# Performance work log

Hardware: AMD Instinct MI355X
Metric: run time of the kernel (lower is better)

## Reference

```python
import jax, jax.numpy as jnp
import numpy as np

DIM = 2048
STATE = 16
BATCH = 2
SEQ = 2048
LN_EPS = 1e-5


def setup_inputs() -> dict:
    key = jax.random.key(0)
    ks = jax.random.split(key, 12)
    d, n = DIM, STATE
    inp = {
        "x": jax.random.normal(ks[0], (BATCH, SEQ, d), dtype=jnp.float32),
        "ln_gamma": jnp.ones((d,), dtype=jnp.float32),
        "ln_beta": jnp.zeros((d,), dtype=jnp.float32),
        # proj_in: Linear(d, 2d) (spectral-normed; weights treated as effective)
        "W_in": jax.random.normal(ks[1], (2 * d, d), dtype=jnp.float32) / np.sqrt(d),
        "b_in": jnp.zeros((2 * d,), dtype=jnp.float32),
        "state_A": jax.random.normal(ks[2], (n, d), dtype=jnp.float32) * 0.01,
        "W_B": jax.random.normal(ks[3], (n, d), dtype=jnp.float32) / np.sqrt(d),
        "b_B": jnp.zeros((n,), dtype=jnp.float32),
        "W_C": jax.random.normal(ks[4], (n, d), dtype=jnp.float32) / np.sqrt(d),
        "b_C": jnp.zeros((n,), dtype=jnp.float32),
        "W_dt": jax.random.normal(ks[5], (d, d), dtype=jnp.float32) / np.sqrt(d),
        "b_dt": jnp.zeros((d,), dtype=jnp.float32),
        "W_out": jax.random.normal(ks[6], (d, d), dtype=jnp.float32) / np.sqrt(d),
        "b_out": jnp.zeros((d,), dtype=jnp.float32),
    }
    return inp


def reference(x, ln_gamma, ln_beta, W_in, b_in, state_A, W_B, b_B, W_C, b_C,
              W_dt, b_dt, W_out, b_out):
    residual = x
    # LayerNorm over last dim
    mu = jnp.mean(x, axis=-1, keepdims=True)
    var = jnp.mean(jnp.square(x - mu), axis=-1, keepdims=True)
    xn = (x - mu) * jax.lax.rsqrt(var + LN_EPS) * ln_gamma + ln_beta
    # input projection and gate split
    xz = jnp.einsum('bsd,ed->bse', xn, W_in) + b_in          # (B,S,2D)
    x_ssm, z = jnp.split(xz, 2, axis=-1)                      # (B,S,D) each
    # dt = clamp(softplus(proj_dt(x_ssm)), max=1.0)
    dt = jnp.minimum(jax.nn.softplus(jnp.einsum('bsd,ed->bse', x_ssm, W_dt) + b_dt), 1.0)
    Bm = jnp.einsum('bsd,nd->bsn', x_ssm, W_B) + b_B          # (B,S,N)
    Cm = jnp.einsum('bsd,nd->bsn', x_ssm, W_C) + b_C          # (B,S,N)
    # A_bar[b,s,n,d] = exp(state_A[n,d] * dt[b,s,d])
    A_bar = jnp.exp(state_A[None, None, :, :] * dt[:, :, None, :])  # (B,S,N,D)
    # y[b,s,d] = sum_n C[b,s,n]*B[b,s,n]*A_bar[b,s,n,d] * x_ssm[b,s,d]
    y = jnp.einsum('bsn,bsnd->bsd', Cm * Bm, A_bar) * x_ssm
    gated = y * jax.nn.silu(z)
    out = jnp.einsum('bsd,ed->bse', gated, W_out) + b_out
    return out + residual
```

## Files before the change

kernel.cpp:

```cpp
#include <hip/hip_runtime.h>

typedef unsigned short u16;
typedef float f32x4 __attribute__((ext_vector_type(4)));
typedef __bf16 bf16x8 __attribute__((ext_vector_type(8)));

__device__ __forceinline__ u16 f2bf(float f) {
    unsigned u = __float_as_uint(f);
    u += 0x7FFFu + ((u >> 16) & 1u);
    return (u16)(u >> 16);
}
__device__ __forceinline__ float b2f(u16 h) {
    return __uint_as_float(((unsigned)h) << 16);
}

__device__ __forceinline__ void async16(const u16* g, u16* l) {
    __builtin_amdgcn_global_load_lds(
        (__attribute__((address_space(1))) void*)(u16*)g,
        (__attribute__((address_space(3))) void*)l,
        16, 0, 0);
}

#define T_TOK 4096
#define DIM   2048

__global__ __launch_bounds__(256) void castln_kernel(const float* __restrict__ W_in,
                                                     u16* __restrict__ wb_in,
                                                     const float* __restrict__ x,
                                                     const float* __restrict__ g,
                                                     const float* __restrict__ b,
                                                     u16* __restrict__ o) {
    __shared__ float s1[4], s2[4];
    int blk = blockIdx.x, tid = threadIdx.x;
    if (blk < 8192) {
        int i = blk * 256 + tid;
        float4 f = ((const float4*)W_in)[i];
        ushort4 u;
        u.x = f2bf(f.x); u.y = f2bf(f.y); u.z = f2bf(f.z); u.w = f2bf(f.w);
        ((ushort4*)wb_in)[i] = u;
        return;
    }
    int t = blk - 8192;
    int wave = tid >> 6, lane = tid & 63;
    size_t base = (size_t)t * DIM;
    int d0 = tid * 8;
    float4 v0 = *(const float4*)(x + base + d0);
    float4 v1 = *(const float4*)(x + base + d0 + 4);
    float v[8] = {v0.x, v0.y, v0.z, v0.w, v1.x, v1.y, v1.z, v1.w};
    float s = 0.f;
#pragma unroll
    for (int j = 0; j < 8; ++j) s += v[j];
#pragma unroll
    for (int o2 = 32; o2; o2 >>= 1) s += __shfl_xor(s, o2);
    if (lane == 0) s1[wave] = s;
    __syncthreads();
    float mu = (s1[0] + s1[1] + s1[2] + s1[3]) * (1.f / DIM);
    float q = 0.f;
#pragma unroll
    for (int j = 0; j < 8; ++j) { float dd = v[j] - mu; q += dd * dd; }
#pragma unroll
    for (int o2 = 32; o2; o2 >>= 1) q += __shfl_xor(q, o2);
    if (lane == 0) s2[wave] = q;
    __syncthreads();
    float var = (s2[0] + s2[1] + s2[2] + s2[3]) * (1.f / DIM);
    float rs = rsqrtf(var + 1e-5f);
    float4 g0 = *(const float4*)(g + d0), g1 = *(const float4*)(g + d0 + 4);
    float4 b0 = *(const float4*)(b + d0), b1 = *(const float4*)(b + d0 + 4);
    float gv[8] = {g0.x, g0.y, g0.z, g0.w, g1.x, g1.y, g1.z, g1.w};
    float bv[8] = {b0.x, b0.y, b0.z, b0.w, b1.x, b1.y, b1.z, b1.w};
    ushort4 r0, r1;
    u16* rp0 = (u16*)&r0; u16* rp1 = (u16*)&r1;
#pragma unroll
    for (int j = 0; j < 4; ++j) {
        rp0[j] = f2bf((v[j] - mu) * rs * gv[j] + bv[j]);
        rp1[j] = f2bf((v[j + 4] - mu) * rs * gv[j + 4] + bv[j + 4]);
    }
    *(ushort4*)(o + base + d0) = r0;
    *(ushort4*)(o + base + d0 + 4) = r1;
}

__global__ __launch_bounds__(256) void cast4_kernel(const float* __restrict__ s0, u16* __restrict__ d0, int n0,
                                                    const float* __restrict__ s1, u16* __restrict__ d1, int n1,
                                                    const float* __restrict__ s2, u16* __restrict__ d2, int n2,
                                                    const float* __restrict__ s3, u16* __restrict__ d3, int n3) {
    int j = blockIdx.x * 256 + threadIdx.x;
    const float* s; u16* d;
    if (j < n0) { s = s0; d = d0; }
    else {
        j -= n0;
        if (j < n1) { s = s1; d = d1; }
        else {
            j -= n1;
            if (j < n2) { s = s2; d = d2; }
            else { j -= n2; if (j >= n3) return; s = s3; d = d3; }
        }
    }
    float4 f = ((const float4*)s)[j];
    ushort4 u;
    u.x = f2bf(f.x); u.y = f2bf(f.y); u.z = f2bf(f.z); u.w = f2bf(f.w);
    ((ushort4*)d)[j] = u;
}

#define GBM 256
#define GBN 256
#define GBK 64

#define WAITV4 asm volatile("s_waitcnt vmcnt(4)" ::: "memory")
#define SBAR() do { __builtin_amdgcn_sched_barrier(0); __builtin_amdgcn_s_barrier(); } while (0)

__global__ __launch_bounds__(512) void gemm_wide(const u16* __restrict__ A,
                                                 const u16* __restrict__ W,
                                                 const float* __restrict__ bias,
                                                 u16* __restrict__ Xs,
                                                 u16* __restrict__ Z, int K) {
    __shared__ __align__(16) u16 lA[2][GBM * GBK];
    __shared__ __align__(16) u16 lB[2][GBN * GBK];
    const int tid = threadIdx.x;
    const int wv = tid >> 6, lane = tid & 63;
    const int quad = lane >> 4, l16 = lane & 15;
    const int wr = wv >> 2, wc = wv & 3;
    const int tM = blockIdx.x * GBM, tN = blockIdx.y * GBN;

    const int srow = tid >> 3;
    const int swz = ((tid & 7) ^ (srow & 7)) * 8;
    const u16* gA = A + (size_t)(tM + srow) * 2048 + swz;
    const u16* gW = W + (size_t)(tN + srow) * 2048 + swz;

#define STAGE_A(BI, KC) do {                                                  \
    _Pragma("unroll") for (int r_ = 0; r_ < 4; ++r_)                          \
      async16(gA + (size_t)r_ * 64 * 2048 + (KC),                             \
              &lA[BI][(r_ * 64 + wv * 8) * GBK]);                             \
  } while (0)
#define STAGE_B(BI, KC) do {                                                  \
    _Pragma("unroll") for (int r_ = 0; r_ < 4; ++r_)                          \
      async16(gW + (size_t)r_ * 64 * 2048 + (KC),                             \
              &lB[BI][(r_ * 64 + wv * 8) * GBK]);                             \
  } while (0)

    int aoff[2][4][2], boff[2][2][2];
#pragma unroll
    for (int qm = 0; qm < 2; ++qm)
#pragma unroll
        for (int mi = 0; mi < 4; ++mi)
#pragma unroll
            for (int h = 0; h < 2; ++h) {
                int row = wr * 128 + (qm * 4 + mi) * 16 + l16;
                aoff[qm][mi][h] = row * GBK + (((h * 4 + quad) ^ (l16 & 7)) * 8);
            }
#pragma unroll
    for (int qn = 0; qn < 2; ++qn)
#pragma unroll
        for (int ni = 0; ni < 2; ++ni)
#pragma unroll
            for (int h = 0; h < 2; ++h) {
                int row = wc * 64 + (qn * 2 + ni) * 16 + l16;
                boff[qn][ni][h] = row * GBK + (((h * 4 + quad) ^ (l16 & 7)) * 8);
            }

    f32x4 acc[8][4] = {};
    bf16x8 af[4][2];

#define PHASE(BI, QM, QN, LOADA, STAGE_STMT, WAIT_STMT) do {                  \
    if (LOADA) {                                                              \
      _Pragma("unroll") for (int mi_ = 0; mi_ < 4; ++mi_)                     \
        _Pragma("unroll") for (int h_ = 0; h_ < 2; ++h_)                      \
          af[mi_][h_] = *(const bf16x8*)&lA[BI][aoff[QM][mi_][h_]];           \
    }                                                                         \
    bf16x8 bfr_[2][2];                                                        \
    _Pragma("unroll") for (int ni_ = 0; ni_ < 2; ++ni_)                       \
      _Pragma("unroll") for (int h_ = 0; h_ < 2; ++h_)                        \
        bfr_[ni_][h_] = *(const bf16x8*)&lB[BI][boff[QN][ni_][h_]];           \
    STAGE_STMT;                                                               \
    SBAR();                                                                   \
    __builtin_amdgcn_s_setprio(1);                                            \
    _Pragma("unroll") for (int mi_ = 0; mi_ < 4; ++mi_)                       \
      _Pragma("unroll") for (int ni_ = 0; ni_ < 2; ++ni_)                     \
        _Pragma("unroll") for (int h_ = 0; h_ < 2; ++h_)                      \
          acc[QM * 4 + mi_][QN * 2 + ni_] =                                   \
              __builtin_amdgcn_mfma_f32_16x16x32_bf16(                        \
                  af[mi_][h_], bfr_[ni_][h_],                                 \
                  acc[QM * 4 + mi_][QN * 2 + ni_], 0, 0, 0);                  \
    __builtin_amdgcn_s_setprio(0);                                            \
    WAIT_STMT;                                                                \
    SBAR();                                                                   \
  } while (0)

    STAGE_A(0, 0);
    STAGE_B(0, 0);
    STAGE_A(1, 64);
    WAITV4;
    SBAR();

    const int NIT = K >> 7;
    for (int it = 0; it < NIT; ++it) {
        const int k1 = it * 128 + 64;
        int kn = it * 128 + 128;
        if (kn > K - 64) kn = K - 64;
        int kn1 = it * 128 + 192;
        if (kn1 > K - 64) kn1 = K - 64;

        PHASE(0, 0, 0, 1, STAGE_B(1, k1), (void)0);
        PHASE(0, 0, 1, 0, (void)0,        (void)0);
        PHASE(0, 1, 0, 1, (void)0,        (void)0);
        PHASE(0, 1, 1, 0, STAGE_A(0, kn), WAITV4);
        PHASE(1, 0, 0, 1, STAGE_B(0, kn), (void)0);
        PHASE(1, 0, 1, 0, (void)0,        (void)0);
        PHASE(1, 1, 0, 1, (void)0,        (void)0);
        PHASE(1, 1, 1, 0, STAGE_A(1, kn1), WAITV4);
    }

    asm volatile("s_waitcnt vmcnt(0)" ::: "memory");

    const bool isb_z = (tN >= 2048);
    u16* dst = isb_z ? Z : Xs;
#pragma unroll
    for (int mi = 0; mi < 8; ++mi) {
#pragma unroll
        for (int ni = 0; ni < 4; ++ni) {
            int col = tN + wc * 64 + ni * 16 + l16;
            float bv = bias[col];
            int ocol = isb_z ? (col - 2048) : col;
#pragma unroll
            for (int r = 0; r < 4; ++r) {
                int row = tM + wr * 128 + mi * 16 + quad * 4 + r;
                dst[(size_t)row * 2048 + ocol] = f2bf(acc[mi][ni][r] + bv);
            }
        }
    }
#undef PHASE
#undef STAGE_A
#undef STAGE_B
}

#define NBM 128
#define NBN 64
#define NBK 64

template <int EPI>
__global__ __launch_bounds__(256) void gemm_nw(const u16* __restrict__ A, int lda,
                                               const u16* __restrict__ W, int ldw,
                                               const float* __restrict__ bias,
                                               const float* __restrict__ resid,
                                               void* __restrict__ C, int ldc, int K,
                                               u16* __restrict__ dots) {
    __shared__ __align__(16) u16 lAB[(NBM + NBN) * NBK];
    const int tid = threadIdx.x;
    const int wave = tid >> 6, lane = tid & 63;
    const int quad = lane >> 4, l16 = lane & 15;
    const int tM = blockIdx.x * NBM;
    const int tN = blockIdx.y * NBN;
    const int wr = wave >> 1, wc = wave & 1;

    const int rowin = tid >> 3;
    const int r3 = rowin & 7;
    const int col8 = ((tid & 7) ^ r3) * 8;
    const u16* gptr[6];
    u16* ldst[6];
#pragma unroll
    for (int i = 0; i < 6; ++i) {
        int trow = i * 32 + rowin;
        const u16* src = (i < 4) ? (A + (size_t)(tM + trow) * lda)
                                 : (W + (size_t)(tN + (trow - NBM)) * ldw);
        gptr[i] = src + col8;
        ldst[i] = &lAB[(i * 32 + wave * 8) * NBK];
    }

    int a_off[2][4], b_off[2][2];
#pragma unroll
    for (int h = 0; h < 2; ++h) {
#pragma unroll
        for (int mi = 0; mi < 4; ++mi)
            a_off[h][mi] = (wr * 64 + mi * 16 + l16) * NBK +
                           (((h * 4 + quad) ^ (l16 & 7)) * 8);
#pragma unroll
        for (int ni = 0; ni < 2; ++ni)
            b_off[h][ni] = (NBM + wc * 32 + ni * 16 + l16) * NBK +
                           (((h * 4 + quad) ^ (l16 & 7)) * 8);
    }

    f32x4 acc[4][2] = {};

    for (int kt = 0; kt < K; kt += NBK) {
#pragma unroll
        for (int i = 0; i < 6; ++i) async16(gptr[i] + kt, ldst[i]);
        __syncthreads();
        bf16x8 af[2][4], bfr[2][2];
#pragma unroll
        for (int h = 0; h < 2; ++h) {
#pragma unroll
            for (int mi = 0; mi < 4; ++mi) af[h][mi] = *(const bf16x8*)&lAB[a_off[h][mi]];
#pragma unroll
            for (int ni = 0; ni < 2; ++ni) bfr[h][ni] = *(const bf16x8*)&lAB[b_off[h][ni]];
        }
#pragma unroll
        for (int h = 0; h < 2; ++h)
#pragma unroll
            for (int mi = 0; mi < 4; ++mi)
#pragma unroll
                for (int ni = 0; ni < 2; ++ni)
                    acc[mi][ni] = __builtin_amdgcn_mfma_f32_16x16x32_bf16(
                        af[h][mi], bfr[h][ni], acc[mi][ni], 0, 0, 0);
        __syncthreads();
    }

#pragma unroll
    for (int mi = 0; mi < 4; ++mi) {
#pragma unroll
        for (int ni = 0; ni < 2; ++ni) {
            int col = tN + wc * 32 + ni * 16 + l16;
            float bv = (EPI == 1 && col >= 2048) ? 0.f : bias[col];
#pragma unroll
            for (int r = 0; r < 4; ++r) {
                int row = tM + wr * 64 + mi * 16 + quad * 4 + r;
                float v = acc[mi][ni][r] + bv;
                if constexpr (EPI == 1) {
                    if (col < 2048) {
                        float sp = (v > 20.f) ? v : log1pf(__expf(v));
                        ((u16*)C)[(size_t)row * ldc + col] = f2bf(fminf(sp, 1.0f));
                    } else if (col < 2080) {
                        dots[(size_t)row * 32 + (col - 2048)] = f2bf(v);
                    }
                } else {
                    size_t idx = (size_t)row * ldc + col;
                    ((float*)C)[idx] = v + resid[idx];
                }
            }
        }
    }
}

__global__ __launch_bounds__(256) void ssm_gate_kernel(const u16* __restrict__ dtb,
                                                       const u16* __restrict__ xsb,
                                                       const u16* __restrict__ zb,
                                                       const float* __restrict__ A,
                                                       const u16* __restrict__ dots,
                                                       const float* __restrict__ bB,
                                                       const float* __restrict__ bC,
                                                       u16* __restrict__ gated) {
    __shared__ float Pl[16];
    int t = blockIdx.x, tid = threadIdx.x;
    if (tid < 16) {
        float Bv = b2f(dots[(size_t)t * 32 + tid]) + bB[tid];
        float Cv = b2f(dots[(size_t)t * 32 + 16 + tid]) + bC[tid];
        Pl[tid] = Bv * Cv;
    }
    __syncthreads();
    size_t dbase = (size_t)t * DIM;
    int d0 = tid * 8;
    ushort4 dth[2], xsh[2], zh[2];
    dth[0] = *(const ushort4*)(dtb + dbase + d0);
    dth[1] = *(const ushort4*)(dtb + dbase + d0 + 4);
    xsh[0] = *(const ushort4*)(xsb + dbase + d0);
    xsh[1] = *(const ushort4*)(xsb + dbase + d0 + 4);
    zh[0]  = *(const ushort4*)(zb + dbase + d0);
    zh[1]  = *(const ushort4*)(zb + dbase + d0 + 4);
    float dtv[8], xsv[8], zv[8];
#pragma unroll
    for (int h = 0; h < 2; ++h) {
        const u16* dp = (const u16*)&dth[h];
        const u16* xp = (const u16*)&xsh[h];
        const u16* zp = (const u16*)&zh[h];
#pragma unroll
        for (int j = 0; j < 4; ++j) {
            dtv[h * 4 + j] = b2f(dp[j]);
            xsv[h * 4 + j] = b2f(xp[j]);
            zv[h * 4 + j]  = b2f(zp[j]);
        }
    }
    float s[8] = {};
#pragma unroll
    for (int n = 0; n < 16; ++n) {
        float4 a0 = *(const float4*)(A + n * DIM + d0);
        float4 a1 = *(const float4*)(A + n * DIM + d0 + 4);
        float pn = Pl[n];
        float av[8] = {a0.x, a0.y, a0.z, a0.w, a1.x, a1.y, a1.z, a1.w};
#pragma unroll
        for (int j = 0; j < 8; ++j) s[j] += pn * __expf(av[j] * dtv[j]);
    }
    ushort4 r0, r1;
    u16* rp0 = (u16*)&r0; u16* rp1 = (u16*)&r1;
#pragma unroll
    for (int j = 0; j < 8; ++j) {
        float y = s[j] * xsv[j];
        float sz = zv[j] * (1.0f / (1.0f + __expf(-zv[j])));
        u16 hv = f2bf(y * sz);
        if (j < 4) rp0[j] = hv; else rp1[j - 4] = hv;
    }
    *(ushort4*)(gated + dbase + d0) = r0;
    *(ushort4*)(gated + dbase + d0 + 4) = r1;
}

extern "C" void kernel_launch(void* const* d_in, const int* in_sizes, int n_in,
                              void* d_out, int out_size, void* d_ws, size_t ws_size,
                              hipStream_t stream) {
    const float* x      = (const float*)d_in[0];
    const float* ln_g   = (const float*)d_in[1];
    const float* ln_b   = (const float*)d_in[2];
    const float* W_in   = (const float*)d_in[3];
    const float* b_in   = (const float*)d_in[4];
    const float* stateA = (const float*)d_in[5];
    const float* W_B    = (const float*)d_in[6];
    const float* b_B    = (const float*)d_in[7];
    const float* W_C    = (const float*)d_in[8];
    const float* b_C    = (const float*)d_in[9];
    const float* W_dt   = (const float*)d_in[10];
    const float* b_dt   = (const float*)d_in[11];
    const float* W_out  = (const float*)d_in[12];
    const float* b_out  = (const float*)d_in[13];

    char* ws = (char*)d_ws;
    u16*   wb_in  = (u16*)(ws);
    u16*   wb_out = (u16*)(ws);
    u16*   xnb    = (u16*)(ws + 16777216);
    u16*   wb_dt  = (u16*)(ws + 16777216);
    u16*   gated  = (u16*)(ws + 16777216);
    u16*   xsb    = (u16*)(ws + 33554432);
    u16*   zb     = (u16*)(ws + 50331648);
    u16*   dtb    = (u16*)(ws + 67108864);
    u16*   dotsb  = (u16*)(ws + 83886080);

    castln_kernel<<<12288, 256, 0, stream>>>(W_in, wb_in, x, ln_g, ln_b, xnb);
    gemm_wide<<<dim3(16, 16), 512, 0, stream>>>(xnb, wb_in, b_in, xsb, zb, 2048);
    cast4_kernel<<<8256, 256, 0, stream>>>(
        W_dt, wb_dt, 1048576,
        W_B,  wb_dt + (size_t)2048 * 2048, 8192,
        W_C,  wb_dt + (size_t)2064 * 2048, 8192,
        W_out, wb_out, 1048576);
    gemm_nw<1><<<dim3(32, 33), 256, 0, stream>>>(xsb, 2048, wb_dt, 2048, b_dt,
                                                 nullptr, dtb, 2048, 2048, dotsb);
    ssm_gate_kernel<<<T_TOK, 256, 0, stream>>>(dtb, xsb, zb, stateA, dotsb,
                                               b_B, b_C, gated);
    gemm_nw<2><<<dim3(32, 32), 256, 0, stream>>>(gated, 2048, wb_out, 2048, b_out,
                                                 x, (float*)d_out, 2048, 2048, nullptr);
}
```

Before: 385.6 us.

## Spread async loads across phases, simplify softplus clamp, batch tokens in SSM gate

The wide GEMM now issues its global-to-LDS loads in half-tile pieces spread over every MFMA phase and waits at vmcnt(2). It also drops the sched_barrier and the pre-compute barrier in each phase, keeping only one barrier per phase. The dt epilogue short-circuits softplus to 1.0 once the clamp is certain and uses fast log/exp. The SSM gate kernel processes 8 tokens per block, keeping state_A in registers so it is not reloaded for every token. Removing the mid-phase barrier risks LDS hazards, since staging into the buffer being read relies on the remaining barriers, and the extra registers may reduce occupancy.

```diff
diff --git a/kernel.cpp b/kernel.cpp
--- a/kernel.cpp
+++ b/kernel.cpp
@@ -104,8 +104,7 @@
 #define GBN 256
 #define GBK 64
 
-#define WAITV4 asm volatile("s_waitcnt vmcnt(4)" ::: "memory")
-#define SBAR() do { __builtin_amdgcn_sched_barrier(0); __builtin_amdgcn_s_barrier(); } while (0)
+#define WAITV2 asm volatile("s_waitcnt vmcnt(2)" ::: "memory")
 
 __global__ __launch_bounds__(512) void gemm_wide(const u16* __restrict__ A,
                                                  const u16* __restrict__ W,
@@ -125,13 +124,13 @@
     const u16* gA = A + (size_t)(tM + srow) * 2048 + swz;
     const u16* gW = W + (size_t)(tN + srow) * 2048 + swz;
 
-#define STAGE_A(BI, KC) do {                                                  \
-    _Pragma("unroll") for (int r_ = 0; r_ < 4; ++r_)                          \
+#define STAGE_AH(BI, KC, H) do {                                              \
+    _Pragma("unroll") for (int r_ = 2 * (H); r_ < 2 * (H) + 2; ++r_)          \
       async16(gA + (size_t)r_ * 64 * 2048 + (KC),                             \
               &lA[BI][(r_ * 64 + wv * 8) * GBK]);                             \
   } while (0)
-#define STAGE_B(BI, KC) do {                                                  \
-    _Pragma("unroll") for (int r_ = 0; r_ < 4; ++r_)                          \
+#define STAGE_BH(BI, KC, H) do {                                              \
+    _Pragma("unroll") for (int r_ = 2 * (H); r_ < 2 * (H) + 2; ++r_)          \
       async16(gW + (size_t)r_ * 64 * 2048 + (KC),                             \
               &lB[BI][(r_ * 64 + wv * 8) * GBK]);                             \
   } while (0)
@@ -170,7 +169,6 @@
       _Pragma("unroll") for (int h_ = 0; h_ < 2; ++h_)                        \
         bfr_[ni_][h_] = *(const bf16x8*)&lB[BI][boff[QN][ni_][h_]];           \
     STAGE_STMT;                                                               \
-    SBAR();                                                                   \
     __builtin_amdgcn_s_setprio(1);                                            \
     _Pragma("unroll") for (int mi_ = 0; mi_ < 4; ++mi_)                       \
       _Pragma("unroll") for (int ni_ = 0; ni_ < 2; ++ni_)                     \
@@ -181,14 +179,16 @@
                   acc[QM * 4 + mi_][QN * 2 + ni_], 0, 0, 0);                  \
     __builtin_amdgcn_s_setprio(0);                                            \
     WAIT_STMT;                                                                \
-    SBAR();                                                                   \
+    __builtin_amdgcn_s_barrier();                                             \
   } while (0)
 
-    STAGE_A(0, 0);
-    STAGE_B(0, 0);
-    STAGE_A(1, 64);
-    WAITV4;
-    SBAR();
+    STAGE_AH(0, 0, 0);
+    STAGE_AH(0, 0, 1);
+    STAGE_BH(0, 0, 0);
+    STAGE_BH(0, 0, 1);
+    STAGE_AH(1, 64, 0);
+    WAITV2;
+    __builtin_amdgcn_s_barrier();
 
     const int NIT = K >> 7;
     for (int it = 0; it < NIT; ++it) {
@@ -198,14 +198,14 @@
         int kn1 = it * 128 + 192;
         if (kn1 > K - 64) kn1 = K - 64;
 
-        PHASE(0, 0, 0, 1, STAGE_B(1, k1), (void)0);
-        PHASE(0, 0, 1, 0, (void)0,        (void)0);
-        PHASE(0, 1, 0, 1, (void)0,        (void)0);
-        PHASE(0, 1, 1, 0, STAGE_A(0, kn), WAITV4);
-        PHASE(1, 0, 0, 1, STAGE_B(0, kn), (void)0);
-        PHASE(1, 0, 1, 0, (void)0,        (void)0);
-        PHASE(1, 1, 0, 1, (void)0,        (void)0);
-        PHASE(1, 1, 1, 0, STAGE_A(1, kn1), WAITV4);
+        PHASE(0, 0, 0, 1, STAGE_AH(1, k1, 1),  (void)0);
+        PHASE(0, 0, 1, 0, STAGE_BH(1, k1, 0),  (void)0);
+        PHASE(0, 1, 0, 1, STAGE_BH(1, k1, 1),  (void)0);
+        PHASE(0, 1, 1, 0, STAGE_AH(0, kn, 0),  WAITV2);
+        PHASE(1, 0, 0, 1, STAGE_AH(0, kn, 1),  (void)0);
+        PHASE(1, 0, 1, 0, STAGE_BH(0, kn, 0),  (void)0);
+        PHASE(1, 1, 0, 1, STAGE_BH(0, kn, 1),  (void)0);
+        PHASE(1, 1, 1, 0, STAGE_AH(1, kn1, 0), WAITV2);
     }
 
     asm volatile("s_waitcnt vmcnt(0)" ::: "memory");
@@ -227,8 +227,8 @@
         }
     }
 #undef PHASE
-#undef STAGE_A
-#undef STAGE_B
+#undef STAGE_AH
+#undef STAGE_BH
 }
 
 #define NBM 128
@@ -314,8 +314,9 @@
                 float v = acc[mi][ni][r] + bv;
                 if constexpr (EPI == 1) {
                     if (col < 2048) {
-                        float sp = (v > 20.f) ? v : log1pf(__expf(v));
-                        ((u16*)C)[(size_t)row * ldc + col] = f2bf(fminf(sp, 1.0f));
+                        float sp = (v > 0.5413f) ? 1.0f
+                                                 : __logf(1.0f + __expf(v));
+                        ((u16*)C)[(size_t)row * ldc + col] = f2bf(sp);
                     } else if (col < 2080) {
                         dots[(size_t)row * 32 + (col - 2048)] = f2bf(v);
                     }
@@ -328,65 +329,72 @@
     }
 }
 
-__global__ __launch_bounds__(256) void ssm_gate_kernel(const u16* __restrict__ dtb,
-                                                       const u16* __restrict__ xsb,
-                                                       const u16* __restrict__ zb,
-                                                       const float* __restrict__ A,
-                                                       const u16* __restrict__ dots,
-                                                       const float* __restrict__ bB,
-                                                       const float* __restrict__ bC,
-                                                       u16* __restrict__ gated) {
-    __shared__ float Pl[16];
-    int t = blockIdx.x, tid = threadIdx.x;
-    if (tid < 16) {
-        float Bv = b2f(dots[(size_t)t * 32 + tid]) + bB[tid];
-        float Cv = b2f(dots[(size_t)t * 32 + 16 + tid]) + bC[tid];
-        Pl[tid] = Bv * Cv;
-    }
-    __syncthreads();
-    size_t dbase = (size_t)t * DIM;
-    int d0 = tid * 8;
-    ushort4 dth[2], xsh[2], zh[2];
-    dth[0] = *(const ushort4*)(dtb + dbase + d0);
-    dth[1] = *(const ushort4*)(dtb + dbase + d0 + 4);
-    xsh[0] = *(const ushort4*)(xsb + dbase + d0);
-    xsh[1] = *(const ushort4*)(xsb + dbase + d0 + 4);
-    zh[0]  = *(const ushort4*)(zb + dbase + d0);
-    zh[1]  = *(const ushort4*)(zb + dbase + d0 + 4);
-    float dtv[8], xsv[8], zv[8];
-#pragma unroll
-    for (int h = 0; h < 2; ++h) {
-        const u16* dp = (const u16*)&dth[h];
-        const u16* xp = (const u16*)&xsh[h];
-        const u16* zp = (const u16*)&zh[h];
-#pragma unroll
-        for (int j = 0; j < 4; ++j) {
-            dtv[h * 4 + j] = b2f(dp[j]);
-            xsv[h * 4 + j] = b2f(xp[j]);
-            zv[h * 4 + j]  = b2f(zp[j]);
-        }
-    }
-    float s[8] = {};
+__global__ __launch_bounds__(256) void ssm_gate2_kernel(const u16* __restrict__ dtb,
+                                                        const u16* __restrict__ xsb,
+                                                        const u16* __restrict__ zb,
+                                                        const float* __restrict__ A,
+                                                        const u16* __restrict__ dots,
+                                                        const float* __restrict__ bB,
+                                                        const float* __restrict__ bC,
+                                                        u16* __restrict__ gated) {
+    __shared__ float Pl[8][16];
+    const int tid = threadIdx.x;
+    const int t0 = blockIdx.x * 8;
+    const int d0 = tid * 8;
+
+    float a[16][8];
 #pragma unroll
     for (int n = 0; n < 16; ++n) {
         float4 a0 = *(const float4*)(A + n * DIM + d0);
         float4 a1 = *(const float4*)(A + n * DIM + d0 + 4);
-        float pn = Pl[n];
-        float av[8] = {a0.x, a0.y, a0.z, a0.w, a1.x, a1.y, a1.z, a1.w};
-#pragma unroll
-        for (int j = 0; j < 8; ++j) s[j] += pn * __expf(av[j] * dtv[j]);
-    }
-    ushort4 r0, r1;
-    u16* rp0 = (u16*)&r0; u16* rp1 = (u16*)&r1;
-#pragma unroll
-    for (int j = 0; j < 8; ++j) {
-        float y = s[j] * xsv[j];
-        float sz = zv[j] * (1.0f / (1.0f + __expf(-zv[j])));
-        u16 hv = f2bf(y * sz);
-        if (j < 4) rp0[j] = hv; else rp1[j - 4] = hv;
-    }
-    *(ushort4*)(gated + dbase + d0) = r0;
-    *(ushort4*)(gated + dbase + d0 + 4) = r1;
+        a[n][0] = a0.x; a[n][1] = a0.y; a[n][2] = a0.z; a[n][3] = a0.w;
+        a[n][4] = a1.x; a[n][5] = a1.y; a[n][6] = a1.z; a[n][7] = a1.w;
+    }
+    if (tid < 128) {
+        int tt = tid >> 4, n = tid & 15;
+        float Bv = b2f(dots[(size_t)(t0 + tt) * 32 + n]) + bB[n];
+        float Cv = b2f(dots[(size_t)(t0 + tt) * 32 + 16 + n]) + bC[n];
+        Pl[tt][n] = Bv * Cv;
+    }
+    __syncthreads();
+
+    for (int tt = 0; tt < 8; ++tt) {
+        size_t dbase = (size_t)(t0 + tt) * DIM;
+        ushort4 dth0 = *(const ushort4*)(dtb + dbase + d0);
+        ushort4 dth1 = *(const ushort4*)(dtb + dbase + d0 + 4);
+        ushort4 xsh0 = *(const ushort4*)(xsb + dbase + d0);
+        ushort4 xsh1 = *(const ushort4*)(xsb + dbase + d0 + 4);
+        ushort4 zh0  = *(const ushort4*)(zb + dbase + d0);
+        ushort4 zh1  = *(const ushort4*)(zb + dbase + d0 + 4);
+        float dtv[8], xsv[8], zv[8];
+        const u16* dp0 = (const u16*)&dth0; const u16* dp1 = (const u16*)&dth1;
+        const u16* xp0 = (const u16*)&xsh0; const u16* xp1 = (const u16*)&xsh1;
+        const u16* zp0 = (const u16*)&zh0;  const u16* zp1 = (const u16*)&zh1;
+#pragma unroll
+        for (int j = 0; j < 4; ++j) {
+            dtv[j] = b2f(dp0[j]); dtv[j + 4] = b2f(dp1[j]);
+            xsv[j] = b2f(xp0[j]); xsv[j + 4] = b2f(xp1[j]);
+            zv[j]  = b2f(zp0[j]); zv[j + 4]  = b2f(zp1[j]);
+        }
+        float s[8] = {};
+#pragma unroll
+        for (int n = 0; n < 16; ++n) {
+            float pn = Pl[tt][n];
+#pragma unroll
+            for (int j = 0; j < 8; ++j) s[j] += pn * __expf(a[n][j] * dtv[j]);
+        }
+        ushort4 r0, r1;
+        u16* rp0 = (u16*)&r0; u16* rp1 = (u16*)&r1;
+#pragma unroll
+        for (int j = 0; j < 8; ++j) {
+            float y = s[j] * xsv[j];
+            float sz = zv[j] * (1.0f / (1.0f + __expf(-zv[j])));
+            u16 hv = f2bf(y * sz);
+            if (j < 4) rp0[j] = hv; else rp1[j - 4] = hv;
+        }
+        *(ushort4*)(gated + dbase + d0) = r0;
+        *(ushort4*)(gated + dbase + d0 + 4) = r1;
+    }
 }
 
 extern "C" void kernel_launch(void* const* d_in, const int* in_sizes, int n_in,
@@ -427,8 +435,8 @@
         W_out, wb_out, 1048576);
     gemm_nw<1><<<dim3(32, 33), 256, 0, stream>>>(xsb, 2048, wb_dt, 2048, b_dt,
                                                  nullptr, dtb, 2048, 2048, dotsb);
-    ssm_gate_kernel<<<T_TOK, 256, 0, stream>>>(dtb, xsb, zb, stateA, dotsb,
-                                               b_B, b_C, gated);
+    ssm_gate2_kernel<<<512, 256, 0, stream>>>(dtb, xsb, zb, stateA, dotsb,
+                                              b_B, b_C, gated);
     gemm_nw<2><<<dim3(32, 32), 256, 0, stream>>>(gated, 2048, wb_out, 2048, b_out,
                                                  x, (float*)d_out, 2048, 2048, nullptr);
 }
```

Result: faster. 355.4 us (-7.8%).
